# Optimization experiments

Measured on AMD Instinct MI355X. Metric: run time of the kernel, lower is better.

Reference implementation:

```python
import jax, jax.numpy as jnp
import numpy as np

D_MODEL = 1024
D_INNER = 2048   # d_model * expansion_factor(2)
D_CONV = 4
N_EXPERTS = 8
TOP_K = 2


def setup_inputs() -> dict:
    key = jax.random.key(0)
    ks = jax.random.split(key, 6)
    s = 0.02
    return {
        "x": jax.random.normal(ks[0], (4, 2048, D_MODEL), jnp.float32),
        "Wr": jax.random.normal(ks[1], (N_EXPERTS, D_MODEL), jnp.float32) * s,
        "br": jnp.zeros((N_EXPERTS,), jnp.float32),
        "Win": jax.random.normal(ks[2], (N_EXPERTS, 2 * D_INNER, D_MODEL), jnp.float32) * s,
        "conv_w": jax.random.normal(ks[3], (N_EXPERTS, D_INNER, D_CONV), jnp.float32) * s,
        "conv_b": jnp.zeros((N_EXPERTS, D_INNER), jnp.float32),
        "Dp": jnp.ones((N_EXPERTS, D_INNER), jnp.float32),
        "Wout": jax.random.normal(ks[4], (N_EXPERTS, D_MODEL, D_INNER), jnp.float32) * s,
    }


def reference(x, Wr, br, Win, conv_w, conv_b, Dp, Wout):
    B, L, C = x.shape
    xf = x.reshape(-1, C)                                   # [N, C]
    logits = xf @ Wr.T + br                                 # [N, E]
    probs = jax.nn.softmax(logits.astype(jnp.float32), axis=-1)
    tw, ti = jax.lax.top_k(probs, TOP_K)                    # [N, k]
    tw = tw / jnp.sum(tw, axis=-1, keepdims=True)
    oh = jax.nn.one_hot(ti, N_EXPERTS, dtype=jnp.float32)   # [N, k, E]
    load = oh.sum(1).mean(0)                                # [E]
    aux_loss = jnp.sum(load * load)
    # per-token combine weight for each expert (sum over top-k slots)
    cw = jnp.einsum('nk,nke->ne', tw, oh)                   # [N, E]
    out = jnp.zeros_like(xf)
    for j in range(N_EXPERTS):
        # Per-token expert (L=1 inside the original loop): causal depthwise
        # conv with left padding reduces to last-tap * x + bias.
        xz = xf @ Win[j].T                                  # [N, 2*D_INNER]
        xi, z = xz[:, :D_INNER], xz[:, D_INNER:]
        xa = jax.nn.silu(xi * conv_w[j, :, -1] + conv_b[j])
        y = xa * Dp[j] * jax.nn.silu(z)
        out = out + cw[:, j:j + 1].astype(xf.dtype) * (y @ Wout[j].T)
    return out.reshape(B, L, C), aux_loss
```

## Files before the change

### kernel.cpp

```cpp
#include <hip/hip_runtime.h>
#include <hip/hip_bf16.h>
#include <stdint.h>

#define NTOK 8192
#define CDIM 1024
#define DIN  2048
#define NEXP 8
#define NSLOT (NTOK * 2)

typedef __bf16 bf16x8 __attribute__((ext_vector_type(8)));
typedef float  f32x4  __attribute__((ext_vector_type(4)));

typedef __attribute__((address_space(1))) const unsigned char GBUF;
typedef __attribute__((address_space(3))) unsigned char LBUF;

__device__ __forceinline__ void gload_lds16(const void* g, void* l) {
    __builtin_amdgcn_global_load_lds((GBUF*)g, (LBUF*)l, 16, 0, 0);
}

__device__ __forceinline__ ushort f2bf(float f) {
    union { float f; unsigned u; } v; v.f = f;
    unsigned u = v.u;
    u += 0x7fffu + ((u >> 16) & 1u);
    return (ushort)(u >> 16);
}
__device__ __forceinline__ float bf2f(ushort u) {
    union { float f; unsigned u; } v; v.u = ((unsigned)u) << 16; return v.f;
}
__device__ __forceinline__ float silu_f(float x) { return x / (1.f + __expf(-x)); }

__device__ __forceinline__ bf16x8 lds_swz(const ushort* L, int row, int kof) {
    return *(const bf16x8*)&L[row * 64 + ((((kof >> 3) ^ row) & 7) << 3)];
}

#define WAITV(N) asm volatile("s_waitcnt vmcnt(" #N ")" ::: "memory")
#define BARR     __builtin_amdgcn_s_barrier()

__global__ void __launch_bounds__(256) k_cvt2(
    const float* __restrict__ srcA, ushort* __restrict__ dstA, int nA4,
    const float* __restrict__ srcB, ushort* __restrict__ dstB, int nB4) {
    int i = blockIdx.x * 256 + threadIdx.x;
    int stride = gridDim.x * 256;
    int ntot = nA4 + nB4;
    for (; i < ntot; i += stride) {
        const float4* s; ushort4* d; int j;
        if (i < nA4) { s = (const float4*)srcA; d = (ushort4*)dstA; j = i; }
        else         { s = (const float4*)srcB; d = (ushort4*)dstB; j = i - nA4; }
        float4 v = s[j];
        ushort4 o;
        o.x = f2bf(v.x); o.y = f2bf(v.y); o.z = f2bf(v.z); o.w = f2bf(v.w);
        d[j] = o;
    }
}

__global__ void __launch_bounds__(256) k_router(
    const float* __restrict__ x, const float* __restrict__ Wr,
    const float* __restrict__ br, int* __restrict__ counts,
    int* __restrict__ tok_e, float* __restrict__ tok_w,
    ushort* __restrict__ xb) {
    int wave = blockIdx.x * 4 + (threadIdx.x >> 6);
    int lane = threadIdx.x & 63;
    const float4* row = (const float4*)(x + (size_t)wave * CDIM);
    ushort4* xrow = (ushort4*)(xb + (size_t)wave * CDIM);
    float acc[NEXP];
#pragma unroll
    for (int e = 0; e < NEXP; ++e) acc[e] = 0.f;
#pragma unroll
    for (int j = 0; j < 4; ++j) {
        float4 v = row[j * 64 + lane];
        ushort4 o;
        o.x = f2bf(v.x); o.y = f2bf(v.y); o.z = f2bf(v.z); o.w = f2bf(v.w);
        xrow[j * 64 + lane] = o;
#pragma unroll
        for (int e = 0; e < NEXP; ++e) {
            float4 w = ((const float4*)(Wr + e * CDIM))[j * 64 + lane];
            acc[e] += v.x * w.x + v.y * w.y + v.z * w.z + v.w * w.w;
        }
    }
#pragma unroll
    for (int off = 32; off > 0; off >>= 1)
#pragma unroll
        for (int e = 0; e < NEXP; ++e) acc[e] += __shfl_xor(acc[e], off, 64);
    if (lane == 0) {
        float l[NEXP];
#pragma unroll
        for (int e = 0; e < NEXP; ++e) l[e] = acc[e] + br[e];
        int i0 = 0; float l0 = l[0];
#pragma unroll
        for (int e = 1; e < NEXP; ++e) if (l[e] > l0) { l0 = l[e]; i0 = e; }
        int i1 = -1; float l1 = -1e30f;
#pragma unroll
        for (int e = 0; e < NEXP; ++e) if (e != i0 && l[e] > l1) { l1 = l[e]; i1 = e; }
        float s  = __expf(l1 - l0);
        float w0 = 1.f / (1.f + s);
        float w1 = 1.f - w0;
        tok_e[wave * 2] = i0; tok_e[wave * 2 + 1] = i1;
        tok_w[wave * 2] = w0; tok_w[wave * 2 + 1] = w1;
        atomicAdd(&counts[i0], 1); atomicAdd(&counts[i1], 1);
    }
}

__global__ void k_scan(const int* __restrict__ counts, int* __restrict__ offsets,
                       int* __restrict__ tileoff, float* __restrict__ out_aux) {
    if (threadIdx.x == 0 && blockIdx.x == 0) {
        int o = 0, tp = 0;
        for (int e = 0; e < NEXP; ++e) {
            offsets[e] = o;
            tileoff[e] = tp;
            o += counts[e];
            tp += (counts[e] + 255) >> 8;
        }
        offsets[NEXP] = o;
        tileoff[NEXP] = tp;
        float aux = 0.f;
        for (int e = 0; e < NEXP; ++e) {
            float ld = (float)counts[e] * (1.f / (float)NTOK);
            aux += ld * ld;
        }
        *out_aux = aux;
    }
}

__global__ void __launch_bounds__(256) k_scatter(
    const int* __restrict__ tok_e, const float* __restrict__ tok_w,
    const int* __restrict__ offsets, int* __restrict__ cursor,
    int* __restrict__ perm_token, int* __restrict__ tok_slot) {
    int t = blockIdx.x * 256 + threadIdx.x;
    if (t >= NTOK) return;
#pragma unroll
    for (int k = 0; k < 2; ++k) {
        int e = tok_e[t * 2 + k];
        int pos = atomicAdd(&cursor[e], 1);
        int s = offsets[e] + pos;
        perm_token[s] = t;
        tok_slot[t * 2 + k] = s;
    }
}

__global__ void __launch_bounds__(512, 2) k_gemm1(
    const ushort* __restrict__ xb, const ushort* __restrict__ Winb,
    const float* __restrict__ conv_w, const float* __restrict__ conv_b,
    const float* __restrict__ Dp, const int* __restrict__ counts,
    const int* __restrict__ offsets, const int* __restrict__ perm_token,
    ushort* __restrict__ y) {
    int h = blockIdx.x;
    int vb = (h & 7) * 160 + (h >> 3);
    int e   = vb / 160;
    int r   = vb % 160;
    int mt0 = r >> 4;
    int nt  = r & 15;
    int cnt = counts[e];
    if (cnt == 0) return;
    int base = offsets[e];
    int mtiles = (cnt + 255) >> 8;
    int n0 = nt * 128;

    __shared__ ushort aL[2][256 * 64];
    __shared__ ushort bL[2][256 * 64];

    int tid = threadIdx.x, lane = tid & 63, w = tid >> 6;
    int Mw = w >> 1, Nw = w & 1;
    const ushort* WinE = Winb + (size_t)e * (2 * DIN) * CDIM;
    int schunk = ((tid & 7) ^ ((tid >> 3) & 7)) << 3;

    uint bsrc[4];
#pragma unroll
    for (int i = 0; i < 4; ++i) {
        int rr = i * 64 + (tid >> 3);
        int grow = (rr < 128) ? (n0 + rr) : (DIN + n0 + (rr - 128));
        bsrc[i] = (uint)grow * CDIM + schunk;
    }

    for (int mt = mt0; mt < mtiles; mt += 10) {
        int rem = cnt - mt * 256;
        uint asrc[4];
#pragma unroll
        for (int i = 0; i < 4; ++i) {
            int rr = i * 64 + (tid >> 3);
            int sidx = base + mt * 256 + (rr < rem ? rr : 0);
            asrc[i] = (uint)perm_token[sidx] * CDIM + schunk;
        }

        f32x4 accXi[4][4], accZ[4][4];
#pragma unroll
        for (int m = 0; m < 4; ++m)
#pragma unroll
            for (int n = 0; n < 4; ++n) {
                accXi[m][n] = f32x4{0.f, 0.f, 0.f, 0.f};
                accZ[m][n]  = f32x4{0.f, 0.f, 0.f, 0.f};
            }

        auto stgA = [&](int bi, int ko, int i, int j) {
            gload_lds16(xb + asrc[i] + ko, &aL[bi][(i * 512 + tid) * 8]);
            gload_lds16(xb + asrc[j] + ko, &aL[bi][(j * 512 + tid) * 8]);
        };
        auto stgB = [&](int bi, int ko, int i, int j) {
            gload_lds16(WinE + bsrc[i] + ko, &bL[bi][(i * 512 + tid) * 8]);
            gload_lds16(WinE + bsrc[j] + ko, &bL[bi][(j * 512 + tid) * 8]);
        };

        bf16x8 af0[4], af1[4], bx[4], bz[4];
        stgA(0, 0, 0, 1); stgA(0, 0, 2, 3); stgB(0, 0, 0, 1); stgB(0, 0, 2, 3);

#pragma unroll 1
        for (int kt = 0; kt < 16; ++kt) {
            int cur = kt & 1, nxt = cur ^ 1;
            const ushort* A = aL[cur];
            const ushort* B = bL[cur];
            int ko = (kt + 1) * 64;
            bool st = kt < 15;
            WAITV(2);
            BARR;
#pragma unroll
            for (int m = 0; m < 4; ++m)
                af0[m] = lds_swz(A, Mw * 64 + m * 16 + (lane & 15), (lane >> 4) * 8);
#pragma unroll
            for (int n = 0; n < 4; ++n)
                bx[n] = lds_swz(B, Nw * 64 + n * 16 + (lane & 15), (lane >> 4) * 8);
            if (st) stgA(nxt, ko, 0, 1);
            __builtin_amdgcn_s_setprio(1);
#pragma unroll
            for (int m = 0; m < 4; ++m)
#pragma unroll
                for (int n = 0; n < 4; ++n)
                    accXi[m][n] = __builtin_amdgcn_mfma_f32_16x16x32_bf16(af0[m], bx[n], accXi[m][n], 0, 0, 0);
            __builtin_amdgcn_s_setprio(0);
            if (st) { WAITV(2); } else { WAITV(0); }
            BARR;
#pragma unroll
            for (int n = 0; n < 4; ++n)
                bz[n] = lds_swz(B, 128 + Nw * 64 + n * 16 + (lane & 15), (lane >> 4) * 8);
            if (st) stgA(nxt, ko, 2, 3);
            __builtin_amdgcn_s_setprio(1);
#pragma unroll
            for (int m = 0; m < 4; ++m)
#pragma unroll
                for (int n = 0; n < 4; ++n)
                    accZ[m][n] = __builtin_amdgcn_mfma_f32_16x16x32_bf16(af0[m], bz[n], accZ[m][n], 0, 0, 0);
            __builtin_amdgcn_s_setprio(0);
            BARR;
#pragma unroll
            for (int m = 0; m < 4; ++m)
                af1[m] = lds_swz(A, Mw * 64 + m * 16 + (lane & 15), 32 + (lane >> 4) * 8);
#pragma unroll
            for (int n = 0; n < 4; ++n)
                bx[n] = lds_swz(B, Nw * 64 + n * 16 + (lane & 15), 32 + (lane >> 4) * 8);
            if (st) stgB(nxt, ko, 0, 1);
            __builtin_amdgcn_s_setprio(1);
#pragma unroll
            for (int m = 0; m < 4; ++m)
#pragma unroll
                for (int n = 0; n < 4; ++n)
                    accXi[m][n] = __builtin_amdgcn_mfma_f32_16x16x32_bf16(af1[m], bx[n], accXi[m][n], 0, 0, 0);
            __builtin_amdgcn_s_setprio(0);
            BARR;
#pragma unroll
            for (int n = 0; n < 4; ++n)
                bz[n] = lds_swz(B, 128 + Nw * 64 + n * 16 + (lane & 15), 32 + (lane >> 4) * 8);
            if (st) stgB(nxt, ko, 2, 3);
            __builtin_amdgcn_s_setprio(1);
#pragma unroll
            for (int m = 0; m < 4; ++m)
#pragma unroll
                for (int n = 0; n < 4; ++n)
                    accZ[m][n] = __builtin_amdgcn_mfma_f32_16x16x32_bf16(af1[m], bz[n], accZ[m][n], 0, 0, 0);
            __builtin_amdgcn_s_setprio(0);
        }
        __syncthreads();

#pragma unroll
        for (int n = 0; n < 4; ++n) {
            int c = n0 + Nw * 64 + n * 16 + (lane & 15);
            float cwl = conv_w[((size_t)e * DIN + c) * 4 + 3];
            float cb  = conv_b[(size_t)e * DIN + c];
            float dp  = Dp[(size_t)e * DIN + c];
#pragma unroll
            for (int m = 0; m < 4; ++m)
#pragma unroll
                for (int q = 0; q < 4; ++q) {
                    int rl = Mw * 64 + m * 16 + (lane >> 4) * 4 + q;
                    if (rl < rem) {
                        int slot = base + mt * 256 + rl;
                        float xi = accXi[m][n][q], z = accZ[m][n][q];
                        float yv = silu_f(xi * cwl + cb) * dp * silu_f(z);
                        y[(size_t)slot * DIN + c] = f2bf(yv);
                    }
                }
        }
        __syncthreads();
    }
}

__global__ void __launch_bounds__(512, 4) k_gemm2(
    const ushort* __restrict__ y, const ushort* __restrict__ Woutb,
    const int* __restrict__ counts, const int* __restrict__ offsets,
    const int* __restrict__ tileoff, ushort* __restrict__ so) {
    __shared__ ushort aL[256 * 64];
    __shared__ ushort bL[128 * 64];

    int tid = threadIdx.x, lane = tid & 63, w = tid >> 6;
    int Mw = w >> 1, Nw = w & 1;
    int schunk = ((tid & 7) ^ ((tid >> 3) & 7)) << 3;

    int ntiles = tileoff[NEXP] * 8;
    int b = blockIdx.x;
    int virt = (b & 7) * 64 + (b >> 3);

    for (int t = virt; t < ntiles; t += 512) {
        int pair = t >> 3, nt = t & 7;
        int e = 0;
#pragma unroll
        for (int k = 1; k < NEXP; ++k) if (pair >= tileoff[k]) e = k;
        int mt = pair - tileoff[e];
        int cnt = counts[e], base = offsets[e];
        int rem = cnt - mt * 256;
        int c0 = nt * 128;
        const ushort* WoutE = Woutb + (size_t)e * CDIM * DIN;

        uint asrc[4], bsrc[2];
#pragma unroll
        for (int i = 0; i < 4; ++i) {
            int rr = i * 64 + (tid >> 3);
            int slot = base + mt * 256 + (rr < rem ? rr : 0);
            asrc[i] = (uint)slot * DIN + schunk;
        }
#pragma unroll
        for (int i = 0; i < 2; ++i) {
            int rr = i * 64 + (tid >> 3);
            bsrc[i] = (uint)(c0 + rr) * DIN + schunk;
        }

        f32x4 acc[4][4];
#pragma unroll
        for (int m = 0; m < 4; ++m)
#pragma unroll
            for (int n = 0; n < 4; ++n) acc[m][n] = f32x4{0.f, 0.f, 0.f, 0.f};

#pragma unroll 1
        for (int kt = 0; kt < 32; ++kt) {
            int ko = kt * 64;
            gload_lds16(y + asrc[0] + ko, &aL[(0 * 512 + tid) * 8]);
            gload_lds16(y + asrc[1] + ko, &aL[(1 * 512 + tid) * 8]);
            gload_lds16(y + asrc[2] + ko, &aL[(2 * 512 + tid) * 8]);
            gload_lds16(y + asrc[3] + ko, &aL[(3 * 512 + tid) * 8]);
            gload_lds16(WoutE + bsrc[0] + ko, &bL[(0 * 512 + tid) * 8]);
            gload_lds16(WoutE + bsrc[1] + ko, &bL[(1 * 512 + tid) * 8]);
            __syncthreads();
#pragma unroll
            for (int kk = 0; kk < 64; kk += 32) {
                int kof = kk + (lane >> 4) * 8;
                bf16x8 af[4], bf[4];
#pragma unroll
                for (int m = 0; m < 4; ++m)
                    af[m] = lds_swz(aL, Mw * 64 + m * 16 + (lane & 15), kof);
#pragma unroll
                for (int n = 0; n < 4; ++n)
                    bf[n] = lds_swz(bL, Nw * 64 + n * 16 + (lane & 15), kof);
                __builtin_amdgcn_s_setprio(1);
#pragma unroll
                for (int m = 0; m < 4; ++m)
#pragma unroll
                    for (int n = 0; n < 4; ++n)
                        acc[m][n] = __builtin_amdgcn_mfma_f32_16x16x32_bf16(af[m], bf[n], acc[m][n], 0, 0, 0);
                __builtin_amdgcn_s_setprio(0);
            }
            __syncthreads();
        }

#pragma unroll
        for (int m = 0; m < 4; ++m)
#pragma unroll
            for (int q = 0; q < 4; ++q) {
                int rl = Mw * 64 + m * 16 + (lane >> 4) * 4 + q;
                if (rl < rem) {
                    int slot = base + mt * 256 + rl;
#pragma unroll
                    for (int n = 0; n < 4; ++n) {
                        int col = c0 + Nw * 64 + n * 16 + (lane & 15);
                        so[(size_t)slot * CDIM + col] = f2bf(acc[m][n][q]);
                    }
                }
            }
        __syncthreads();
    }
}

__global__ void __launch_bounds__(256) k_combine(
    const ushort* __restrict__ so, const int* __restrict__ tok_slot,
    const float* __restrict__ tok_w, float* __restrict__ out) {
    int i = blockIdx.x * 256 + threadIdx.x;
    int t  = i >> 7;
    int c8 = (i & 127) << 3;
    int s0 = tok_slot[t * 2], s1 = tok_slot[t * 2 + 1];
    float w0 = tok_w[t * 2],  w1 = tok_w[t * 2 + 1];
    uint4 a = *(const uint4*)(so + (size_t)s0 * CDIM + c8);
    uint4 b = *(const uint4*)(so + (size_t)s1 * CDIM + c8);
    const ushort* au = (const ushort*)&a;
    const ushort* bu = (const ushort*)&b;
    float4 o0, o1;
    o0.x = w0 * bf2f(au[0]) + w1 * bf2f(bu[0]);
    o0.y = w0 * bf2f(au[1]) + w1 * bf2f(bu[1]);
    o0.z = w0 * bf2f(au[2]) + w1 * bf2f(bu[2]);
    o0.w = w0 * bf2f(au[3]) + w1 * bf2f(bu[3]);
    o1.x = w0 * bf2f(au[4]) + w1 * bf2f(bu[4]);
    o1.y = w0 * bf2f(au[5]) + w1 * bf2f(bu[5]);
    o1.z = w0 * bf2f(au[6]) + w1 * bf2f(bu[6]);
    o1.w = w0 * bf2f(au[7]) + w1 * bf2f(bu[7]);
    float4* dst = (float4*)(out + (size_t)t * CDIM + c8);
    dst[0] = o0; dst[1] = o1;
}

extern "C" void kernel_launch(void* const* d_in, const int* in_sizes, int n_in,
                              void* d_out, int out_size, void* d_ws, size_t ws_size,
                              hipStream_t stream) {
    const float* x      = (const float*)d_in[0];
    const float* Wr     = (const float*)d_in[1];
    const float* br     = (const float*)d_in[2];
    const float* Win    = (const float*)d_in[3];
    const float* conv_w = (const float*)d_in[4];
    const float* conv_b = (const float*)d_in[5];
    const float* Dp     = (const float*)d_in[6];
    const float* Wout   = (const float*)d_in[7];
    float* out = (float*)d_out;

    char* ws = (char*)d_ws;
    int*    counts     = (int*)(ws + 0);
    int*    offsets    = (int*)(ws + 64);
    int*    cursor     = (int*)(ws + 128);
    int*    tileoff    = (int*)(ws + 192);
    int*    tok_e      = (int*)(ws + 4096);
    float*  tok_w      = (float*)(ws + 4096 + 1 * 65536);
    int*    perm_token = (int*)(ws + 4096 + 2 * 65536);
    int*    tok_slot   = (int*)(ws + 4096 + 3 * 65536);
    const size_t MB = 1u << 20;
    ushort* y     = (ushort*)(ws + MB);
    ushort* xb    = (ushort*)(ws + MB + 67108864);
    ushort* winb  = (ushort*)(ws + MB + 67108864 + 16777216);
    ushort* woutb = (ushort*)(ws + MB + 67108864 + 16777216 + 67108864);
    ushort* so    = winb;

    hipMemsetAsync(ws, 0, 256, stream);

    k_cvt2<<<3072, 256, 0, stream>>>(Win,  winb,  NEXP * 2 * DIN * CDIM / 4,
                                     Wout, woutb, NEXP * CDIM * DIN / 4);

    k_router<<<NTOK / 4, 256, 0, stream>>>(x, Wr, br, counts, tok_e, tok_w, xb);
    k_scan<<<1, 64, 0, stream>>>(counts, offsets, tileoff, out + (size_t)NTOK * CDIM);
    k_scatter<<<NTOK / 256, 256, 0, stream>>>(tok_e, tok_w, offsets, cursor, perm_token, tok_slot);

    k_gemm1<<<NEXP * 160, 512, 0, stream>>>(xb, winb, conv_w, conv_b, Dp,
                                            counts, offsets, perm_token, y);
    k_gemm2<<<512, 512, 0, stream>>>(y, woutb, counts, offsets, tileoff, so);
    k_combine<<<NTOK * 128 / 256, 256, 0, stream>>>(so, tok_slot, tok_w, out);
}
```

Before: 623.9 us.

## Fuse weighted combine into GEMM2 epilogue via atomics and drop scan kernel

Removes the separate scan kernel by recomputing expert offsets and tile offsets from counts inside the scatter, gemm1 and gemm2 kernels, with the aux loss written by the scatter kernel. The combine kernel is also removed: gemm2 now scales each output by its routing weight and atomically adds fp32 results straight into the output, which is zeroed by a memset first. This avoids the bf16 intermediate write, the reread and two kernel launches, but adds a full-output memset and float atomics, whose summation order is nondeterministic.

```diff
diff --git a/kernel.cpp b/kernel.cpp
--- a/kernel.cpp
+++ b/kernel.cpp
@@ -100,40 +100,32 @@
     }
 }
 
-__global__ void k_scan(const int* __restrict__ counts, int* __restrict__ offsets,
-                       int* __restrict__ tileoff, float* __restrict__ out_aux) {
-    if (threadIdx.x == 0 && blockIdx.x == 0) {
-        int o = 0, tp = 0;
-        for (int e = 0; e < NEXP; ++e) {
-            offsets[e] = o;
-            tileoff[e] = tp;
-            o += counts[e];
-            tp += (counts[e] + 255) >> 8;
-        }
-        offsets[NEXP] = o;
-        tileoff[NEXP] = tp;
-        float aux = 0.f;
-        for (int e = 0; e < NEXP; ++e) {
-            float ld = (float)counts[e] * (1.f / (float)NTOK);
-            aux += ld * ld;
-        }
-        *out_aux = aux;
-    }
-}
-
 __global__ void __launch_bounds__(256) k_scatter(
     const int* __restrict__ tok_e, const float* __restrict__ tok_w,
-    const int* __restrict__ offsets, int* __restrict__ cursor,
-    int* __restrict__ perm_token, int* __restrict__ tok_slot) {
+    const int* __restrict__ counts, int* __restrict__ cursor,
+    int* __restrict__ perm_token, float* __restrict__ perm_w,
+    float* __restrict__ out_aux) {
     int t = blockIdx.x * 256 + threadIdx.x;
     if (t >= NTOK) return;
+    int off[NEXP]; int o = 0;
+#pragma unroll
+    for (int k = 0; k < NEXP; ++k) { off[k] = o; o += counts[k]; }
+    if (t == 0) {
+        float aux = 0.f;
+#pragma unroll
+        for (int k = 0; k < NEXP; ++k) {
+            float ld = (float)counts[k] * (1.f / (float)NTOK);
+            aux += ld * ld;
+        }
+        *out_aux = aux;
+    }
 #pragma unroll
     for (int k = 0; k < 2; ++k) {
         int e = tok_e[t * 2 + k];
         int pos = atomicAdd(&cursor[e], 1);
-        int s = offsets[e] + pos;
+        int s = off[e] + pos;
         perm_token[s] = t;
-        tok_slot[t * 2 + k] = s;
+        perm_w[s] = tok_w[t * 2 + k];
     }
 }
 
@@ -141,17 +133,18 @@
     const ushort* __restrict__ xb, const ushort* __restrict__ Winb,
     const float* __restrict__ conv_w, const float* __restrict__ conv_b,
     const float* __restrict__ Dp, const int* __restrict__ counts,
-    const int* __restrict__ offsets, const int* __restrict__ perm_token,
-    ushort* __restrict__ y) {
+    const int* __restrict__ perm_token, ushort* __restrict__ y) {
     int h = blockIdx.x;
     int vb = (h & 7) * 160 + (h >> 3);
     int e   = vb / 160;
     int r   = vb % 160;
     int mt0 = r >> 4;
     int nt  = r & 15;
+    int base = 0;
+#pragma unroll
+    for (int k = 0; k < NEXP; ++k) if (k < e) base += counts[k];
     int cnt = counts[e];
     if (cnt == 0) return;
-    int base = offsets[e];
     int mtiles = (cnt + 255) >> 8;
     int n0 = nt * 128;
 
@@ -293,8 +286,8 @@
 
 __global__ void __launch_bounds__(512, 4) k_gemm2(
     const ushort* __restrict__ y, const ushort* __restrict__ Woutb,
-    const int* __restrict__ counts, const int* __restrict__ offsets,
-    const int* __restrict__ tileoff, ushort* __restrict__ so) {
+    const int* __restrict__ counts, const int* __restrict__ perm_token,
+    const float* __restrict__ perm_w, float* __restrict__ out) {
     __shared__ ushort aL[256 * 64];
     __shared__ ushort bL[128 * 64];
 
@@ -302,7 +295,18 @@
     int Mw = w >> 1, Nw = w & 1;
     int schunk = ((tid & 7) ^ ((tid >> 3) & 7)) << 3;
 
-    int ntiles = tileoff[NEXP] * 8;
+    int cnts[NEXP], off[NEXP], tp[NEXP + 1];
+    {
+        int o = 0, t = 0;
+#pragma unroll
+        for (int k = 0; k < NEXP; ++k) {
+            cnts[k] = counts[k];
+            off[k] = o; o += cnts[k];
+            tp[k] = t; t += (cnts[k] + 255) >> 8;
+        }
+        tp[NEXP] = t;
+    }
+    int ntiles = tp[NEXP] * 8;
     int b = blockIdx.x;
     int virt = (b & 7) * 64 + (b >> 3);
 
@@ -310,9 +314,9 @@
         int pair = t >> 3, nt = t & 7;
         int e = 0;
 #pragma unroll
-        for (int k = 1; k < NEXP; ++k) if (pair >= tileoff[k]) e = k;
-        int mt = pair - tileoff[e];
-        int cnt = counts[e], base = offsets[e];
+        for (int k = 1; k < NEXP; ++k) if (pair >= tp[k]) e = k;
+        int mt = pair - tp[e];
+        int cnt = cnts[e], base = off[e];
         int rem = cnt - mt * 256;
         int c0 = nt * 128;
         const ushort* WoutE = Woutb + (size_t)e * CDIM * DIN;
@@ -374,40 +378,17 @@
                 int rl = Mw * 64 + m * 16 + (lane >> 4) * 4 + q;
                 if (rl < rem) {
                     int slot = base + mt * 256 + rl;
+                    int tok = perm_token[slot];
+                    float wgt = perm_w[slot];
 #pragma unroll
                     for (int n = 0; n < 4; ++n) {
                         int col = c0 + Nw * 64 + n * 16 + (lane & 15);
-                        so[(size_t)slot * CDIM + col] = f2bf(acc[m][n][q]);
+                        atomicAdd(&out[(size_t)tok * CDIM + col], wgt * acc[m][n][q]);
                     }
                 }
             }
         __syncthreads();
     }
-}
-
-__global__ void __launch_bounds__(256) k_combine(
-    const ushort* __restrict__ so, const int* __restrict__ tok_slot,
-    const float* __restrict__ tok_w, float* __restrict__ out) {
-    int i = blockIdx.x * 256 + threadIdx.x;
-    int t  = i >> 7;
-    int c8 = (i & 127) << 3;
-    int s0 = tok_slot[t * 2], s1 = tok_slot[t * 2 + 1];
-    float w0 = tok_w[t * 2],  w1 = tok_w[t * 2 + 1];
-    uint4 a = *(const uint4*)(so + (size_t)s0 * CDIM + c8);
-    uint4 b = *(const uint4*)(so + (size_t)s1 * CDIM + c8);
-    const ushort* au = (const ushort*)&a;
-    const ushort* bu = (const ushort*)&b;
-    float4 o0, o1;
-    o0.x = w0 * bf2f(au[0]) + w1 * bf2f(bu[0]);
-    o0.y = w0 * bf2f(au[1]) + w1 * bf2f(bu[1]);
-    o0.z = w0 * bf2f(au[2]) + w1 * bf2f(bu[2]);
-    o0.w = w0 * bf2f(au[3]) + w1 * bf2f(bu[3]);
-    o1.x = w0 * bf2f(au[4]) + w1 * bf2f(bu[4]);
-    o1.y = w0 * bf2f(au[5]) + w1 * bf2f(bu[5]);
-    o1.z = w0 * bf2f(au[6]) + w1 * bf2f(bu[6]);
-    o1.w = w0 * bf2f(au[7]) + w1 * bf2f(bu[7]);
-    float4* dst = (float4*)(out + (size_t)t * CDIM + c8);
-    dst[0] = o0; dst[1] = o1;
 }
 
 extern "C" void kernel_launch(void* const* d_in, const int* in_sizes, int n_in,
@@ -425,31 +406,29 @@
 
     char* ws = (char*)d_ws;
     int*    counts     = (int*)(ws + 0);
-    int*    offsets    = (int*)(ws + 64);
     int*    cursor     = (int*)(ws + 128);
-    int*    tileoff    = (int*)(ws + 192);
     int*    tok_e      = (int*)(ws + 4096);
     float*  tok_w      = (float*)(ws + 4096 + 1 * 65536);
     int*    perm_token = (int*)(ws + 4096 + 2 * 65536);
-    int*    tok_slot   = (int*)(ws + 4096 + 3 * 65536);
+    float*  perm_w     = (float*)(ws + 4096 + 3 * 65536);
     const size_t MB = 1u << 20;
     ushort* y     = (ushort*)(ws + MB);
     ushort* xb    = (ushort*)(ws + MB + 67108864);
     ushort* winb  = (ushort*)(ws + MB + 67108864 + 16777216);
     ushort* woutb = (ushort*)(ws + MB + 67108864 + 16777216 + 67108864);
-    ushort* so    = winb;
 
     hipMemsetAsync(ws, 0, 256, stream);
+    hipMemsetAsync(d_out, 0, (size_t)out_size * sizeof(float), stream);
 
     k_cvt2<<<3072, 256, 0, stream>>>(Win,  winb,  NEXP * 2 * DIN * CDIM / 4,
                                      Wout, woutb, NEXP * CDIM * DIN / 4);
 
     k_router<<<NTOK / 4, 256, 0, stream>>>(x, Wr, br, counts, tok_e, tok_w, xb);
-    k_scan<<<1, 64, 0, stream>>>(counts, offsets, tileoff, out + (size_t)NTOK * CDIM);
-    k_scatter<<<NTOK / 256, 256, 0, stream>>>(tok_e, tok_w, offsets, cursor, perm_token, tok_slot);
+    k_scatter<<<NTOK / 256, 256, 0, stream>>>(tok_e, tok_w, counts, cursor,
+                                              perm_token, perm_w,
+                                              out + (size_t)NTOK * CDIM);
 
     k_gemm1<<<NEXP * 160, 512, 0, stream>>>(xb, winb, conv_w, conv_b, Dp,
-                                            counts, offsets, perm_token, y);
-    k_gemm2<<<512, 512, 0, stream>>>(y, woutb, counts, offsets, tileoff, so);
-    k_combine<<<NTOK * 128 / 256, 256, 0, stream>>>(so, tok_slot, tok_w, out);
-}
+                                            counts, perm_token, y);
+    k_gemm2<<<512, 512, 0, stream>>>(y, woutb, counts, perm_token, perm_w, out);
+}
```

Result: slower. 658.5 us (+5.5%).
